# Kernel tuning notes

Measured on AMD Instinct MI355X. Metric: run time of the kernel, lower is better.

Reference implementation:

```python
import jax, jax.numpy as jnp
import numpy as np

E = 384        # number of edges
HID = 128      # hidden_dim
NH = 8         # num_heads
DH = HID // NH # head_dim = 16
NR = 64        # num_radial
CUTOFF = 10.0
AIN = 2 * DH + NR + 1  # attention MLP input dim = 97


def _xavier(key, fan_in, fan_out):
    a = np.sqrt(6.0 / (fan_in + fan_out))
    return jax.random.uniform(key, (fan_in, fan_out), jnp.float32, -a, a)


def setup_inputs() -> dict:
    key = jax.random.key(0)
    ks = jax.random.split(key, 16)
    return {
        "edge_features": jax.random.normal(ks[0], (E, HID), jnp.float32),
        "edge_coords": jax.random.normal(ks[1], (E, 3), jnp.float32),
        "edge_mask": jnp.zeros((E, E), jnp.float32),  # 0 = connected
        "wq": _xavier(ks[2], HID, HID),
        "wk": _xavier(ks[3], HID, HID),
        "wv": _xavier(ks[4], HID, HID),
        "rbf_centers": jnp.linspace(0.0, CUTOFF, NR).astype(jnp.float32),
        "rbf_widths": jnp.full((NR,), 0.5, jnp.float32),
        "a_w1": _xavier(ks[5], AIN, HID), "a_b1": jnp.zeros((HID,), jnp.float32),
        "a_w2": _xavier(ks[6], HID, HID), "a_b2": jnp.zeros((HID,), jnp.float32),
        "a_w3": _xavier(ks[7], HID, NH),  "a_b3": jnp.zeros((NH,), jnp.float32),
        "g_w1": _xavier(ks[8], DH, HID),  "g_b1": jnp.zeros((HID,), jnp.float32),
        "g_w2": _xavier(ks[9], HID, 1),   "g_b2": jnp.zeros((1,), jnp.float32),
        "wo": _xavier(ks[10], HID, HID),  "bo": jnp.zeros((HID,), jnp.float32),
        "ln_g": jnp.ones((HID,), jnp.float32),
        "ln_b": jnp.zeros((HID,), jnp.float32),
        "edge_index": jax.random.randint(ks[11], (2, E), 0, E, jnp.int64) if jax.config.jax_enable_x64 else jax.random.randint(ks[11], (2, E), 0, E, jnp.int32),
    }


def reference(edge_features, edge_coords, edge_mask,
              wq, wk, wv, rbf_centers, rbf_widths,
              a_w1, a_b1, a_w2, a_b2, a_w3, a_b3,
              g_w1, g_b1, g_w2, g_b2, wo, bo, ln_g, ln_b,
              edge_index):
    silu = jax.nn.silu
    n = edge_features.shape[0]

    q = (edge_features @ wq).reshape(n, NH, DH)
    k = (edge_features @ wk).reshape(n, NH, DH)
    v = (edge_features @ wv).reshape(n, NH, DH)

    # pairwise geometry [E, E, ...]
    coord_diff = edge_coords[:, None, :] - edge_coords[None, :, :]
    dist = jnp.linalg.norm(coord_diff, axis=-1) + 1e-8
    dist = jnp.clip(dist, 1e-8, 1e8)
    dot = jnp.clip(jnp.sum(edge_coords[:, None, :] * edge_coords[None, :, :], -1),
                   -1e8, 1e8)
    d = dist[..., None]                               # [E, E, 1]
    rbf = jnp.exp(-rbf_widths * (d - rbf_centers) ** 2) * (d <= CUTOFF).astype(jnp.float32)

    feats = []
    coords = edge_coords
    for h in range(NH):  # structural loop over fixed num_heads
        qh = jnp.broadcast_to(q[:, h, None, :], (n, n, DH))
        kh = jnp.broadcast_to(k[None, :, h, :], (n, n, DH))
        ai = jnp.concatenate([qh, kh, rbf, dot[..., None]], -1)  # [E, E, 97]
        x = silu(ai @ a_w1 + a_b1)
        x = silu(x @ a_w2 + a_b2)
        scores = (x @ a_w3 + a_b3)[:, :, h] + edge_mask
        scores = jnp.clip(scores, -1e9, 1e9)
        attn = jax.nn.softmax(scores, axis=-1)
        attn = jnp.nan_to_num(attn, nan=0.0, posinf=1.0, neginf=0.0)
        vh = v[:, h, :]
        feats.append(attn @ vh)
        # coord gate from v_head of the query edge, broadcast over keys
        gates = jax.nn.sigmoid(silu(vh @ g_w1 + g_b1) @ g_w2 + g_b2)  # [E, 1]
        coords = coords + jnp.einsum('ij,ijc->ic', attn * gates, coord_diff) / NH

    upd = jnp.concatenate(feats, -1)             # [E, hidden]
    y = edge_features + upd @ wo + bo            # residual + out_proj
    mu = jnp.mean(y, -1, keepdims=True)
    var = jnp.var(y, -1, keepdims=True)
    out_f = (y - mu) / jnp.sqrt(var + 1e-5) * ln_g + ln_b
    return out_f, coords
```

## Files before the change

### kernel.cpp

```cpp
#include <hip/hip_runtime.h>
#include <hip/hip_bf16.h>

#define N 384
#define HIDN 128
#define NHD 8
#define DHD 16
#define NRB 64
#define CUTF 10.0f

#define WS_V 0
#define WS_QPB (WS_V + N*HIDN)
#define WS_KPB (WS_QPB + N*NHD*HIDN/2)
#define WS_GATE (WS_KPB + N*NHD*HIDN/2)
#define WS_UPD (WS_GATE + N*NHD)
#define WS_SCORES (WS_UPD + N*HIDN)
#define WS_W2BF (WS_SCORES + NHD*N*N)

typedef short bf16x8 __attribute__((ext_vector_type(8)));
typedef float floatx4 __attribute__((ext_vector_type(4)));
#define MFMA16(a, b, c) __builtin_amdgcn_mfma_f32_16x16x32_bf16(a, b, c, 0, 0, 0)

__device__ __forceinline__ float siluf(float x) { return x / (1.0f + __expf(-x)); }
__device__ __forceinline__ float silu_fast(float x) {
    return x * __builtin_amdgcn_rcpf(1.0f + __expf(-x));
}
__device__ __forceinline__ short f2bf(float f) {
    unsigned int b = __float_as_uint(f);
    unsigned int r = (b + 0x7fffu + ((b >> 16) & 1u)) >> 16;
    return (short)r;
}
__device__ __forceinline__ float bf2f(short s) {
    return __uint_as_float(((unsigned int)(unsigned short)s) << 16);
}
__device__ __forceinline__ unsigned int cvt_pk_bf16(float lo, float hi) {
    unsigned int r;
    asm("v_cvt_pk_bf16_f32 %0, %1, %2" : "=v"(r) : "v"(lo), "v"(hi));
    return r;
}
__device__ __forceinline__ float wave_sum(float v) {
    for (int o = 32; o; o >>= 1) v += __shfl_down(v, o, 64);
    return v;
}

__global__ __launch_bounds__(128) void k_pre(const float* __restrict__ ef,
    const float* __restrict__ wq, const float* __restrict__ wk, const float* __restrict__ wv,
    const float* __restrict__ aw1, const float* __restrict__ aw2,
    const float* __restrict__ gw1, const float* __restrict__ gb1,
    const float* __restrict__ gw2, const float* __restrict__ gb2,
    float* __restrict__ v, unsigned short* __restrict__ Qpb,
    unsigned short* __restrict__ Kpb, float* __restrict__ gates,
    unsigned short* __restrict__ w2bf) {
    __shared__ float sE[HIDN], sQ[HIDN], sK[HIDN], sV[HIDN];
    __shared__ float sRed[2];
    int i = blockIdx.x, t = threadIdx.x;
    if (i < HIDN) w2bf[(size_t)i * HIDN + t] = (unsigned short)f2bf(aw2[t * HIDN + i]);
    sE[t] = ef[i * HIDN + t];
    __syncthreads();
    float aq = 0.f, ak = 0.f, av = 0.f;
#pragma unroll 8
    for (int c = 0; c < HIDN; c++) {
        float e = sE[c];
        aq += e * wq[c * HIDN + t];
        ak += e * wk[c * HIDN + t];
        av += e * wv[c * HIDN + t];
    }
    v[i * HIDN + t] = av;
    sQ[t] = aq; sK[t] = ak; sV[t] = av;
    __syncthreads();
    for (int h = 0; h < NHD; h++) {
        float accq = 0.f, acck = 0.f;
#pragma unroll
        for (int d = 0; d < DHD; d++) {
            accq += sQ[h * DHD + d] * aw1[d * HIDN + t];
            acck += sK[h * DHD + d] * aw1[(DHD + d) * HIDN + t];
        }
        Qpb[(i * NHD + h) * HIDN + t] = (unsigned short)f2bf(accq);
        Kpb[(i * NHD + h) * HIDN + t] = (unsigned short)f2bf(acck);
        float tt = gb1[t];
#pragma unroll
        for (int d = 0; d < DHD; d++) tt += sV[h * DHD + d] * gw1[d * HIDN + t];
        float contrib = siluf(tt) * gw2[t];
        float s = wave_sum(contrib);
        if ((t & 63) == 0) sRed[t >> 6] = s;
        __syncthreads();
        if (t == 0) gates[i * NHD + h] = 1.0f / (1.0f + __expf(-(sRed[0] + sRed[1] + gb2[0])));
        __syncthreads();
    }
}

#define OFF_W2T 0
#define OFF_QPB 32768
#define OFF_SDD 34816
#define OFF_RBF 34944
#define OFF_R   39040
#define SMEM_SZ 55936

__global__ __launch_bounds__(512, 4) void k_scores_mfma(
    const float* __restrict__ coords, const float* __restrict__ mask,
    const float* __restrict__ centers, const float* __restrict__ widths,
    const float* __restrict__ aw1, const float* __restrict__ ab1,
    const float* __restrict__ ab2,
    const float* __restrict__ aw3, const float* __restrict__ ab3,
    const unsigned short* __restrict__ Qpb, const unsigned short* __restrict__ Kpb,
    const unsigned short* __restrict__ w2bf,
    float* __restrict__ scores) {
    __shared__ __align__(16) char smem[SMEM_SZ];
    const int t = threadIdx.x;
    const int lane = t & 63;
    const int w = t >> 6;
    const int l15 = lane & 15;
    const int quad = lane >> 4;
    const int i = blockIdx.y;
    const int jb = blockIdx.x * 128;

    {
        const uint4* src = (const uint4*)w2bf;
        for (int idx = t; idx < 2048; idx += 512) {
            int row = idx >> 4, slot = idx & 15;
            *(uint4*)(smem + OFF_W2T + row * 256 + ((slot * 16) ^ ((row & 7) << 4))) = src[idx];
        }
    }
    if (t < 128) {
        ((uint4*)(smem + OFF_QPB))[t] = ((const uint4*)(Qpb + (size_t)i * NHD * HIDN))[t];
    }
    const int c0 = w * 16 + l15;
    bf16x8 BW1[2];
#pragma unroll
    for (int ks = 0; ks < 2; ks++) {
        bf16x8 a;
#pragma unroll
        for (int e = 0; e < 8; e++) {
            int r = ks * 32 + quad * 8 + e;
            a[e] = f2bf(aw1[(32 + r) * HIDN + c0]);
        }
        BW1[ks] = a;
    }
    const float b1v = ab1[c0];
    const float w1dv = aw1[96 * HIDN + c0];
    const float ab3v = ab3[w];
    float b2r[8], w3r[8];
#pragma unroll
    for (int ct = 0; ct < 8; ct++) {
        b2r[ct] = ab2[ct * 16 + l15];
        w3r[ct] = aw3[(ct * 16 + l15) * NHD + w];
    }
    const float cr = centers[t & 63], rwd = widths[t & 63];
    const float cix = coords[i * 3], ciy = coords[i * 3 + 1], ciz = coords[i * 3 + 2];
    __syncthreads();

    for (int ch = 0; ch < 4; ch++) {
        const int j0 = jb + ch * 32;
        {
            int r = t & 63;
#pragma unroll
            for (int p = 0; p < 4; p++) {
                int j = w + p * 8;
                int jj = j0 + j;
                float jx = coords[jj * 3], jy = coords[jj * 3 + 1], jz = coords[jj * 3 + 2];
                float dx = cix - jx, dy = ciy - jy, dz = ciz - jz;
                float dist = sqrtf(dx * dx + dy * dy + dz * dz) + 1e-8f;
                dist = fminf(fmaxf(dist, 1e-8f), 1e8f);
                float dd = dist - cr;
                float val = (dist <= CUTF) ? __expf(-rwd * dd * dd) : 0.0f;
                *(short*)(smem + OFF_RBF + j * 128 + ((r * 2) ^ ((j & 7) << 4))) = f2bf(val);
            }
            if (t < 32) {
                int jj = j0 + t;
                float jx = coords[jj * 3], jy = coords[jj * 3 + 1], jz = coords[jj * 3 + 2];
                float dot = fminf(fmaxf(cix * jx + ciy * jy + ciz * jz, -1e8f), 1e8f);
                *(float*)(smem + OFF_SDD + t * 4) = dot;
            }
        }
        __syncthreads();
#pragma unroll
        for (int jt = 0; jt < 2; jt++) {
            int jl = jt * 16 + l15;
            int sw = (jl & 7) << 4;
            bf16x8 ra0 = *(const bf16x8*)(smem + OFF_RBF + jl * 128 + ((quad * 16) ^ sw));
            bf16x8 ra1 = *(const bf16x8*)(smem + OFF_RBF + jl * 128 + ((64 + quad * 16) ^ sw));
            floatx4 acc;
#pragma unroll
            for (int r = 0; r < 4; r++) {
                float dotv = *(const float*)(smem + OFF_SDD + (jt * 16 + quad * 4 + r) * 4);
                acc[r] = b1v + dotv * w1dv;
            }
            acc = MFMA16(ra0, BW1[0], acc);
            acc = MFMA16(ra1, BW1[1], acc);
#pragma unroll
            for (int r = 0; r < 4; r++)
                *(float*)(smem + OFF_R + (jt * 16 + quad * 4 + r) * 528 + c0 * 4) = acc[r];
        }
        __syncthreads();
        {
            bf16x8 A2[2][4];
#pragma unroll
            for (int f = 0; f < 4; f++) {
                const int c8 = f * 32 + quad * 8;
                bf16x8 qp = *(const bf16x8*)(smem + OFF_QPB + (w * HIDN + c8) * 2);
#pragma unroll
                for (int jt = 0; jt < 2; jt++) {
                    const int jl = jt * 16 + l15;
                    bf16x8 kp = *(const bf16x8*)(Kpb + ((size_t)(j0 + jl) * NHD + w) * HIDN + c8);
                    const char* rbase = smem + OFF_R + jl * 528 + c8 * 4;
                    float4 r0 = *(const float4*)(rbase);
                    float4 r1 = *(const float4*)(rbase + 16);
                    float xs[8] = {r0.x, r0.y, r0.z, r0.w, r1.x, r1.y, r1.z, r1.w};
                    union { unsigned int u[4]; bf16x8 v; } uu;
#pragma unroll
                    for (int e2 = 0; e2 < 4; e2++) {
                        float xa = silu_fast(bf2f(kp[2 * e2])     + bf2f(qp[2 * e2])     + xs[2 * e2]);
                        float xb = silu_fast(bf2f(kp[2 * e2 + 1]) + bf2f(qp[2 * e2 + 1]) + xs[2 * e2 + 1]);
                        uu.u[e2] = cvt_pk_bf16(xa, xb);
                    }
                    A2[jt][f] = uu.v;
                }
            }
            float part0[4] = {0.f, 0.f, 0.f, 0.f};
            float part1[4] = {0.f, 0.f, 0.f, 0.f};
#pragma unroll 2
            for (int ct = 0; ct < 8; ct++) {
                const int rw2 = ct * 16 + l15;
                const char* wb = smem + OFF_W2T + rw2 * 256;
                const int sw = (rw2 & 7) << 4;
                bf16x8 b0 = *(const bf16x8*)(wb + ((quad * 16) ^ sw));
                bf16x8 b1 = *(const bf16x8*)(wb + ((64 + quad * 16) ^ sw));
                bf16x8 b2 = *(const bf16x8*)(wb + ((128 + quad * 16) ^ sw));
                bf16x8 b3 = *(const bf16x8*)(wb + ((192 + quad * 16) ^ sw));
                float bb = b2r[ct], ww = w3r[ct];
                floatx4 acc0 = {bb, bb, bb, bb};
                acc0 = MFMA16(A2[0][0], b0, acc0);
                acc0 = MFMA16(A2[0][1], b1, acc0);
                acc0 = MFMA16(A2[0][2], b2, acc0);
                acc0 = MFMA16(A2[0][3], b3, acc0);
                floatx4 acc1 = {bb, bb, bb, bb};
                acc1 = MFMA16(A2[1][0], b0, acc1);
                acc1 = MFMA16(A2[1][1], b1, acc1);
                acc1 = MFMA16(A2[1][2], b2, acc1);
                acc1 = MFMA16(A2[1][3], b3, acc1);
#pragma unroll
                for (int r = 0; r < 4; r++) {
                    part0[r] += silu_fast(acc0[r]) * ww;
                    part1[r] += silu_fast(acc1[r]) * ww;
                }
            }
#pragma unroll
            for (int off = 1; off < 16; off <<= 1) {
#pragma unroll
                for (int r = 0; r < 4; r++) {
                    part0[r] += __shfl_xor(part0[r], off, 64);
                    part1[r] += __shfl_xor(part1[r], off, 64);
                }
            }
            if (l15 == 0) {
#pragma unroll
                for (int r = 0; r < 4; r++) {
                    int j = quad * 4 + r;
                    float s = part0[r] + ab3v + mask[(size_t)i * N + j0 + j];
                    s = fminf(fmaxf(s, -1e9f), 1e9f);
                    scores[((size_t)w * N + i) * N + j0 + j] = s;
                    int j2 = 16 + quad * 4 + r;
                    float s2 = part1[r] + ab3v + mask[(size_t)i * N + j0 + j2];
                    s2 = fminf(fmaxf(s2, -1e9f), 1e9f);
                    scores[((size_t)w * N + i) * N + j0 + j2] = s2;
                }
            }
        }
        __syncthreads();
    }
}

__global__ __launch_bounds__(256) void k_attn2(
    const float* __restrict__ scores, const float* __restrict__ v,
    const float* __restrict__ gates, const float* __restrict__ coords,
    float* __restrict__ upd, float* __restrict__ out) {
    __shared__ float sA[4][N];
    __shared__ float sCrd[N * 3];
    __shared__ float sC[NHD][3];
    int i = blockIdx.x, t = threadIdx.x, w = t >> 6, lane = t & 63;
    for (int idx = t; idx < N * 3; idx += 256) sCrd[idx] = coords[idx];
    float cix = coords[i * 3], ciy = coords[i * 3 + 1], ciz = coords[i * 3 + 2];
    __syncthreads();
    for (int hh = 0; hh < 2; hh++) {
        int h = hh * 4 + w;
        const float* srow = scores + ((size_t)h * N + i) * N;
        float s[6];
#pragma unroll
        for (int p = 0; p < 6; p++) s[p] = srow[lane + 64 * p];
        float m = s[0];
#pragma unroll
        for (int p = 1; p < 6; p++) m = fmaxf(m, s[p]);
        for (int off = 1; off < 64; off <<= 1) m = fmaxf(m, __shfl_xor(m, off, 64));
        float e[6], sum = 0.f;
#pragma unroll
        for (int p = 0; p < 6; p++) { e[p] = __expf(s[p] - m); sum += e[p]; }
        for (int off = 1; off < 64; off <<= 1) sum += __shfl_xor(sum, off, 64);
        float inv = 1.0f / sum;
#pragma unroll
        for (int p = 0; p < 6; p++) sA[w][lane + 64 * p] = e[p] * inv;
        __syncthreads();
        int d4 = lane & 3, grp = lane >> 2;
        float4 f4 = {0.f, 0.f, 0.f, 0.f};
        for (int j = grp; j < N; j += 16) {
            float a = sA[w][j];
            float4 vv = *(const float4*)(v + j * HIDN + h * DHD + d4 * 4);
            f4.x += a * vv.x; f4.y += a * vv.y; f4.z += a * vv.z; f4.w += a * vv.w;
        }
#pragma unroll
        for (int off = 4; off < 64; off <<= 1) {
            f4.x += __shfl_xor(f4.x, off, 64);
            f4.y += __shfl_xor(f4.y, off, 64);
            f4.z += __shfl_xor(f4.z, off, 64);
            f4.w += __shfl_xor(f4.w, off, 64);
        }
        if (lane < 4) *(float4*)(upd + i * HIDN + h * DHD + lane * 4) = f4;
        float cx = 0.f, cy = 0.f, cz = 0.f;
#pragma unroll
        for (int p = 0; p < 6; p++) {
            int j = lane + 64 * p;
            float a = sA[w][j];
            cx += a * (cix - sCrd[j * 3]);
            cy += a * (ciy - sCrd[j * 3 + 1]);
            cz += a * (ciz - sCrd[j * 3 + 2]);
        }
        for (int off = 1; off < 64; off <<= 1) {
            cx += __shfl_xor(cx, off, 64);
            cy += __shfl_xor(cy, off, 64);
            cz += __shfl_xor(cz, off, 64);
        }
        if (lane == 0) {
            float g = gates[i * NHD + h] * (1.0f / NHD);
            sC[h][0] = g * cx; sC[h][1] = g * cy; sC[h][2] = g * cz;
        }
        __syncthreads();
    }
    if (t < 3) {
        float acc = coords[i * 3 + t];
#pragma unroll
        for (int h = 0; h < NHD; h++) acc += sC[h][t];
        out[N * HIDN + i * 3 + t] = acc;
    }
}

__global__ __launch_bounds__(128) void k_out(
    const float* __restrict__ ef, const float* __restrict__ upd,
    const float* __restrict__ wo, const float* __restrict__ bo,
    const float* __restrict__ lng, const float* __restrict__ lnb,
    float* __restrict__ out) {
    __shared__ float sU[HIDN];
    __shared__ float sR[2];
    int i = blockIdx.x, c = threadIdx.x;
    sU[c] = upd[i * HIDN + c];
    __syncthreads();
    float y = ef[i * HIDN + c] + bo[c];
#pragma unroll 8
    for (int cp = 0; cp < HIDN; cp++) y += sU[cp] * wo[cp * HIDN + c];
    float s = wave_sum(y);
    if ((c & 63) == 0) sR[c >> 6] = s;
    __syncthreads();
    float mu = (sR[0] + sR[1]) * (1.0f / HIDN);
    __syncthreads();
    float dv = y - mu;
    float s2 = wave_sum(dv * dv);
    if ((c & 63) == 0) sR[c >> 6] = s2;
    __syncthreads();
    float var = (sR[0] + sR[1]) * (1.0f / HIDN);
    out[i * HIDN + c] = dv * rsqrtf(var + 1e-5f) * lng[c] + lnb[c];
}

extern "C" void kernel_launch(void* const* d_in, const int* in_sizes, int n_in,
                              void* d_out, int out_size, void* d_ws, size_t ws_size,
                              hipStream_t stream) {
    const float* ef      = (const float*)d_in[0];
    const float* coords  = (const float*)d_in[1];
    const float* mask    = (const float*)d_in[2];
    const float* wq      = (const float*)d_in[3];
    const float* wk      = (const float*)d_in[4];
    const float* wv      = (const float*)d_in[5];
    const float* centers = (const float*)d_in[6];
    const float* widths  = (const float*)d_in[7];
    const float* aw1     = (const float*)d_in[8];
    const float* ab1     = (const float*)d_in[9];
    const float* aw2     = (const float*)d_in[10];
    const float* ab2     = (const float*)d_in[11];
    const float* aw3     = (const float*)d_in[12];
    const float* ab3     = (const float*)d_in[13];
    const float* gw1     = (const float*)d_in[14];
    const float* gb1     = (const float*)d_in[15];
    const float* gw2     = (const float*)d_in[16];
    const float* gb2     = (const float*)d_in[17];
    const float* wo      = (const float*)d_in[18];
    const float* bo      = (const float*)d_in[19];
    const float* lng     = (const float*)d_in[20];
    const float* lnb     = (const float*)d_in[21];
    float* ws = (float*)d_ws;
    float* v      = ws + WS_V;
    unsigned short* Qpb = (unsigned short*)(ws + WS_QPB);
    unsigned short* Kpb = (unsigned short*)(ws + WS_KPB);
    float* gates  = ws + WS_GATE;
    float* upd    = ws + WS_UPD;
    float* scores = ws + WS_SCORES;
    unsigned short* w2bf = (unsigned short*)(ws + WS_W2BF);
    float* out = (float*)d_out;

    k_pre<<<N, 128, 0, stream>>>(ef, wq, wk, wv, aw1, aw2, gw1, gb1, gw2, gb2, v, Qpb, Kpb, gates, w2bf);
    k_scores_mfma<<<dim3(3, N), 512, 0, stream>>>(
        coords, mask, centers, widths, aw1, ab1, ab2, aw3, ab3, Qpb, Kpb, w2bf, scores);
    k_attn2<<<N, 256, 0, stream>>>(scores, v, gates, coords, upd, out);
    k_out<<<N, 128, 0, stream>>>(ef, upd, wo, bo, lng, lnb, out);
}
```

Baseline: 277.8 us.

## Double-buffer RBF stage and prefetch K projections in scores kernel

Restructures the scores kernel loop so the RBF/dot computation for the next 32-key chunk runs while the current chunk's second MLP layer executes, using double-buffered shared memory for RBF and dot values. K-projection rows for the next chunk are prefetched into registers ahead of use. The b2 and w3 vectors move from per-thread registers into shared memory to relieve register pressure. This cuts one barrier per chunk and hides global-load latency, but raises shared-memory use per block, which could reduce occupancy at 4 blocks per CU.

```diff
diff --git a/kernel.cpp b/kernel.cpp
--- a/kernel.cpp
+++ b/kernel.cpp
@@ -91,9 +91,11 @@
 #define OFF_W2T 0
 #define OFF_QPB 32768
 #define OFF_SDD 34816
-#define OFF_RBF 34944
-#define OFF_R   39040
-#define SMEM_SZ 55936
+#define OFF_RBF 35072
+#define OFF_R   43264
+#define OFF_B2  60160
+#define OFF_W3  60672
+#define SMEM_SZ 64768
 
 __global__ __launch_bounds__(512, 4) void k_scores_mfma(
     const float* __restrict__ coords, const float* __restrict__ mask,
@@ -122,6 +124,11 @@
     }
     if (t < 128) {
         ((uint4*)(smem + OFF_QPB))[t] = ((const uint4*)(Qpb + (size_t)i * NHD * HIDN))[t];
+        *(float*)(smem + OFF_B2 + t * 4) = ab2[t];
+    }
+    for (int idx = t; idx < HIDN * NHD; idx += 512) {
+        int c = idx >> 3, h = idx & 7;
+        *(float*)(smem + OFF_W3 + (h * 128 + c) * 4) = aw3[idx];
     }
     const int c0 = w * 16 + l15;
     bf16x8 BW1[2];
@@ -138,59 +145,69 @@
     const float b1v = ab1[c0];
     const float w1dv = aw1[96 * HIDN + c0];
     const float ab3v = ab3[w];
-    float b2r[8], w3r[8];
-#pragma unroll
-    for (int ct = 0; ct < 8; ct++) {
-        b2r[ct] = ab2[ct * 16 + l15];
-        w3r[ct] = aw3[(ct * 16 + l15) * NHD + w];
-    }
-    const float cr = centers[t & 63], rwd = widths[t & 63];
+    const float cr = centers[lane], rwd = widths[lane];
     const float cix = coords[i * 3], ciy = coords[i * 3 + 1], ciz = coords[i * 3 + 2];
-    __syncthreads();
-
-    for (int ch = 0; ch < 4; ch++) {
-        const int j0 = jb + ch * 32;
-        {
-            int r = t & 63;
-#pragma unroll
-            for (int p = 0; p < 4; p++) {
-                int j = w + p * 8;
-                int jj = j0 + j;
-                float jx = coords[jj * 3], jy = coords[jj * 3 + 1], jz = coords[jj * 3 + 2];
-                float dx = cix - jx, dy = ciy - jy, dz = ciz - jz;
-                float dist = sqrtf(dx * dx + dy * dy + dz * dz) + 1e-8f;
-                dist = fminf(fmaxf(dist, 1e-8f), 1e8f);
-                float dd = dist - cr;
-                float val = (dist <= CUTF) ? __expf(-rwd * dd * dd) : 0.0f;
-                *(short*)(smem + OFF_RBF + j * 128 + ((r * 2) ^ ((j & 7) << 4))) = f2bf(val);
-            }
-            if (t < 32) {
-                int jj = j0 + t;
-                float jx = coords[jj * 3], jy = coords[jj * 3 + 1], jz = coords[jj * 3 + 2];
-                float dot = fminf(fmaxf(cix * jx + ciy * jy + ciz * jz, -1e8f), 1e8f);
-                *(float*)(smem + OFF_SDD + t * 4) = dot;
-            }
-        }
-        __syncthreads();
+
+    auto a_phase = [&](int ci, int bb) {
+        const int j0 = jb + ci * 32;
+        char* rb = smem + OFF_RBF + bb * 4096;
+#pragma unroll
+        for (int p = 0; p < 4; p++) {
+            int j = w + p * 8;
+            int jj = j0 + j;
+            float jx = coords[jj * 3], jy = coords[jj * 3 + 1], jz = coords[jj * 3 + 2];
+            float dx = cix - jx, dy = ciy - jy, dz = ciz - jz;
+            float dist = sqrtf(dx * dx + dy * dy + dz * dz) + 1e-8f;
+            dist = fminf(fmaxf(dist, 1e-8f), 1e8f);
+            float dd = dist - cr;
+            float val = (dist <= CUTF) ? __expf(-rwd * dd * dd) : 0.0f;
+            *(short*)(rb + j * 128 + ((lane * 2) ^ ((j & 7) << 4))) = f2bf(val);
+        }
+        if (t < 32) {
+            int jj = j0 + t;
+            float jx = coords[jj * 3], jy = coords[jj * 3 + 1], jz = coords[jj * 3 + 2];
+            float dot = fminf(fmaxf(cix * jx + ciy * jy + ciz * jz, -1e8f), 1e8f);
+            *(float*)(smem + OFF_SDD + bb * 128 + t * 4) = dot;
+        }
+    };
+
+    auto b_phase = [&](int bb) {
+        const char* rb = smem + OFF_RBF + bb * 4096;
+        const float* sdd = (const float*)(smem + OFF_SDD + bb * 128);
 #pragma unroll
         for (int jt = 0; jt < 2; jt++) {
             int jl = jt * 16 + l15;
             int sw = (jl & 7) << 4;
-            bf16x8 ra0 = *(const bf16x8*)(smem + OFF_RBF + jl * 128 + ((quad * 16) ^ sw));
-            bf16x8 ra1 = *(const bf16x8*)(smem + OFF_RBF + jl * 128 + ((64 + quad * 16) ^ sw));
+            bf16x8 ra0 = *(const bf16x8*)(rb + jl * 128 + ((quad * 16) ^ sw));
+            bf16x8 ra1 = *(const bf16x8*)(rb + jl * 128 + ((64 + quad * 16) ^ sw));
             floatx4 acc;
 #pragma unroll
-            for (int r = 0; r < 4; r++) {
-                float dotv = *(const float*)(smem + OFF_SDD + (jt * 16 + quad * 4 + r) * 4);
-                acc[r] = b1v + dotv * w1dv;
-            }
+            for (int r = 0; r < 4; r++)
+                acc[r] = b1v + sdd[jt * 16 + quad * 4 + r] * w1dv;
             acc = MFMA16(ra0, BW1[0], acc);
             acc = MFMA16(ra1, BW1[1], acc);
 #pragma unroll
             for (int r = 0; r < 4; r++)
                 *(float*)(smem + OFF_R + (jt * 16 + quad * 4 + r) * 528 + c0 * 4) = acc[r];
         }
-        __syncthreads();
+    };
+
+    a_phase(0, 0);
+    bf16x8 KPF[2][4];
+#pragma unroll
+    for (int jt = 0; jt < 2; jt++) {
+        const unsigned short* kr = Kpb + ((size_t)(jb + jt * 16 + l15) * NHD + w) * HIDN + quad * 8;
+#pragma unroll
+        for (int f = 0; f < 4; f++) KPF[jt][f] = *(const bf16x8*)(kr + f * 32);
+    }
+    __syncthreads();
+    b_phase(0);
+    __syncthreads();
+
+    for (int ch = 0; ch < 4; ch++) {
+        const int j0 = jb + ch * 32;
+        const int nb = (ch + 1) & 1;
+        if (ch < 3) a_phase(ch + 1, nb);
         {
             bf16x8 A2[2][4];
 #pragma unroll
@@ -200,7 +217,7 @@
 #pragma unroll
                 for (int jt = 0; jt < 2; jt++) {
                     const int jl = jt * 16 + l15;
-                    bf16x8 kp = *(const bf16x8*)(Kpb + ((size_t)(j0 + jl) * NHD + w) * HIDN + c8);
+                    bf16x8 kp = KPF[jt][f];
                     const char* rbase = smem + OFF_R + jl * 528 + c8 * 4;
                     float4 r0 = *(const float4*)(rbase);
                     float4 r1 = *(const float4*)(rbase + 16);
@@ -213,6 +230,15 @@
                         uu.u[e2] = cvt_pk_bf16(xa, xb);
                     }
                     A2[jt][f] = uu.v;
+                }
+            }
+            if (ch < 3) {
+                const int j0n = jb + (ch + 1) * 32;
+#pragma unroll
+                for (int jt = 0; jt < 2; jt++) {
+                    const unsigned short* kr = Kpb + ((size_t)(j0n + jt * 16 + l15) * NHD + w) * HIDN + quad * 8;
+#pragma unroll
+                    for (int f = 0; f < 4; f++) KPF[jt][f] = *(const bf16x8*)(kr + f * 32);
                 }
             }
             float part0[4] = {0.f, 0.f, 0.f, 0.f};
@@ -226,7 +252,8 @@
                 bf16x8 b1 = *(const bf16x8*)(wb + ((64 + quad * 16) ^ sw));
                 bf16x8 b2 = *(const bf16x8*)(wb + ((128 + quad * 16) ^ sw));
                 bf16x8 b3 = *(const bf16x8*)(wb + ((192 + quad * 16) ^ sw));
-                float bb = b2r[ct], ww = w3r[ct];
+                float bb = *(const float*)(smem + OFF_B2 + rw2 * 4);
+                float ww = *(const float*)(smem + OFF_W3 + (w * 128 + rw2) * 4);
                 floatx4 acc0 = {bb, bb, bb, bb};
                 acc0 = MFMA16(A2[0][0], b0, acc0);
                 acc0 = MFMA16(A2[0][1], b1, acc0);
@@ -266,6 +293,10 @@
             }
         }
         __syncthreads();
+        if (ch < 3) {
+            b_phase(nb);
+            __syncthreads();
+        }
     }
 }
 
```

After: 298.8 us. 7.6% more time.
